# Optimization experiments

Measured on AMD Instinct MI355X. Metric: run time of the kernel, lower is better.

The kernel has to match this reference:

```python
import jax, jax.numpy as jnp
import numpy as np

B, S, H, KV, D, HID = 1, 2048, 32, 8, 128, 4096
SCALE = D ** -0.5
EPS = 1e-5
QMAX = 127.0  # 8-bit symmetric fake quant


def fake_quant(x):
    # per-tensor symmetric int8 fake quantization with straight-through estimator
    s = jnp.maximum(jnp.max(jnp.abs(x)), 1e-5) / QMAX
    q = jnp.clip(jnp.round(x / s), -QMAX - 1.0, QMAX) * s
    return x + jax.lax.stop_gradient(q - x)


def rms_norm(x, w):
    xf = x.astype(jnp.float32)
    var = jnp.mean(xf * xf, axis=-1, keepdims=True)
    return (xf * jax.lax.rsqrt(var + EPS)).astype(x.dtype) * w


def rotate_half(x):
    h = x.shape[-1] // 2
    return jnp.concatenate([-x[..., h:], x[..., :h]], axis=-1)


def qlinear(x, W):
    # QuantLinear: fake-quant activation and weight, then matmul (no bias)
    return fake_quant(x) @ fake_quant(W).T


def setup_inputs() -> dict:
    key = jax.random.key(0)
    ks = jax.random.split(key, 5)
    hidden_states = jax.random.normal(ks[0], (B, S, HID), jnp.float32)
    # RoPE tables
    inv_freq = 1.0 / (10000.0 ** (np.arange(0, D, 2, dtype=np.float32) / D))
    freqs = np.outer(np.arange(S, dtype=np.float32), inv_freq)  # [S, D/2]
    emb = np.concatenate([freqs, freqs], axis=-1)  # [S, D]
    cos = jnp.asarray(np.cos(emb))[None]  # [1,S,D]
    sin = jnp.asarray(np.sin(emb))[None]
    # causal additive mask [1,1,S,S]
    mask = jnp.where(np.tril(np.ones((S, S), dtype=bool)), 0.0, -1e9).astype(jnp.float32)[None, None]
    Wq = jax.random.normal(ks[1], (H * D, HID), jnp.float32) * 0.02
    Wk = jax.random.normal(ks[2], (KV * D, HID), jnp.float32) * 0.02
    Wv = jax.random.normal(ks[3], (KV * D, HID), jnp.float32) * 0.02
    Wo = jax.random.normal(ks[4], (HID, H * D), jnp.float32) * 0.02
    q_norm_w = jnp.ones((D,), jnp.float32)
    k_norm_w = jnp.ones((D,), jnp.float32)
    return dict(hidden_states=hidden_states, cos=cos, sin=sin, attention_mask=mask,
                Wq=Wq, Wk=Wk, Wv=Wv, Wo=Wo, q_norm_w=q_norm_w, k_norm_w=k_norm_w)


def reference(hidden_states, cos, sin, attention_mask, Wq, Wk, Wv, Wo, q_norm_w, k_norm_w):
    b, s, _ = hidden_states.shape
    q = qlinear(hidden_states, Wq).reshape(b, s, H, D).transpose(0, 2, 1, 3)   # [B,H,S,D]
    k = qlinear(hidden_states, Wk).reshape(b, s, KV, D).transpose(0, 2, 1, 3)  # [B,KV,S,D]
    v = qlinear(hidden_states, Wv).reshape(b, s, KV, D).transpose(0, 2, 1, 3)
    q = rms_norm(q, q_norm_w)
    k = rms_norm(k, k_norm_w)
    c = cos[:, None]  # unsqueeze head dim -> [1,1,S,D]
    sn = sin[:, None]
    q = q * c + rotate_half(q) * sn
    k = k * c + rotate_half(k) * sn
    n_rep = H // KV
    k = jnp.repeat(k, n_rep, axis=1)  # [B,H,S,D]
    v = jnp.repeat(v, n_rep, axis=1)
    # fake-quant around QK^T
    q = fake_quant(q)
    k = fake_quant(k)
    scores = jnp.einsum('bhqd,bhkd->bhqk', q, k) * SCALE + attention_mask
    p = jax.nn.softmax(scores.astype(jnp.float32), axis=-1).astype(q.dtype)
    # fake-quant around PV
    p = fake_quant(p)
    v = fake_quant(v)
    out = jnp.einsum('bhqk,bhkd->bhqd', p, v)
    out = out.transpose(0, 2, 1, 3).reshape(b, s, H * D)
    return qlinear(out, Wo)
```

## Files before the change

### kernel.cpp

```cpp
#include <hip/hip_runtime.h>
#include <hip/hip_bf16.h>
#include <math.h>
#include <stdint.h>

#define S_LEN 2048
#define NH    32
#define NKV   8
#define HD    128
#define HIDD  4096

typedef unsigned short u16;
typedef __attribute__((ext_vector_type(4))) int i32x4;

#define GLD16(g, l) __builtin_amdgcn_global_load_lds( \
    (const __attribute__((address_space(1))) void*)(g), \
    (__attribute__((address_space(3))) void*)(l), 16, 0, 0)


__device__ __forceinline__ float slot_scale(const unsigned* slot) {
    return fmaxf(__uint_as_float(*slot), 1e-5f) / 127.0f;
}

__device__ __forceinline__ float exp2_fast(float x) {
    float r; asm("v_exp_f32 %0, %1" : "=v"(r) : "v"(x)); return r;
}
__device__ __forceinline__ float log2_fast(float x) {
    float r; asm("v_log_f32 %0, %1" : "=v"(r) : "v"(x)); return r;
}

__device__ __forceinline__ int qint(float x, float s) {
    float q = rintf(x / s);
    q = fminf(fmaxf(q, -128.0f), 127.0f);
    return (int)q;
}

__device__ __forceinline__ void block_amax_atomic(float m, unsigned* slot) {
    __shared__ float wmax[8];
    const int lane = threadIdx.x & 63;
    const int wid  = threadIdx.x >> 6;
    const int nw   = blockDim.x >> 6;
    #pragma unroll
    for (int o = 32; o; o >>= 1) m = fmaxf(m, __shfl_xor(m, o));
    if (lane == 0) wmax[wid] = m;
    __syncthreads();
    if (threadIdx.x == 0) {
        float bm = wmax[0];
        for (int i = 1; i < nw; ++i) bm = fmaxf(bm, wmax[i]);
        atomicMax(slot, __float_as_uint(bm));
    }
}

struct Amax5Args { const float* p[5]; size_t n4[5]; };
__global__ __launch_bounds__(256) void absmax5_kernel(Amax5Args a, unsigned* slots) {
    const int t = blockIdx.y;
    const float4* x4 = (const float4*)a.p[t];
    const size_t n4 = a.n4[t];
    size_t i = (size_t)blockIdx.x * blockDim.x + threadIdx.x;
    size_t stride = (size_t)gridDim.x * blockDim.x;
    float m = 0.0f;
    for (; i < n4; i += stride) {
        float4 v = x4[i];
        m = fmaxf(m, fmaxf(fmaxf(fabsf(v.x), fabsf(v.y)), fmaxf(fabsf(v.z), fabsf(v.w))));
    }
    block_amax_atomic(m, slots + t);
}

struct Quant5Args { const float* p[5]; char* o[5]; size_t n4[5]; };
__global__ __launch_bounds__(256) void quant5_kernel(Quant5Args a, const unsigned* slots) {
    const int t = blockIdx.y;
    float s = slot_scale(slots + t);
    const float4* x4 = (const float4*)a.p[t];
    unsigned* o4 = (unsigned*)a.o[t];
    const size_t n4 = a.n4[t];
    size_t i = (size_t)blockIdx.x * blockDim.x + threadIdx.x;
    size_t stride = (size_t)gridDim.x * blockDim.x;
    for (; i < n4; i += stride) {
        float4 v = x4[i];
        unsigned o = (unsigned)(qint(v.x, s) & 255)
                   | ((unsigned)(qint(v.y, s) & 255) << 8)
                   | ((unsigned)(qint(v.z, s) & 255) << 16)
                   | ((unsigned)(qint(v.w, s) & 255) << 24);
        o4[i] = o;
    }
}

__global__ __launch_bounds__(256) void quant_kernel(const float* __restrict__ x,
                                                    size_t n4, const unsigned* slot,
                                                    char* __restrict__ out) {
    float s = slot_scale(slot);
    size_t i = (size_t)blockIdx.x * blockDim.x + threadIdx.x;
    size_t stride = (size_t)gridDim.x * blockDim.x;
    const float4* x4 = (const float4*)x;
    unsigned* o4 = (unsigned*)out;
    for (; i < n4; i += stride) {
        float4 v = x4[i];
        unsigned o = (unsigned)(qint(v.x, s) & 255)
                   | ((unsigned)(qint(v.y, s) & 255) << 8)
                   | ((unsigned)(qint(v.z, s) & 255) << 16)
                   | ((unsigned)(qint(v.w, s) & 255) << 24);
        o4[i] = o;
    }
}

__device__ __forceinline__ void gemm_body(const char* __restrict__ A,
                                          const char* __restrict__ B,
                                          float* __restrict__ C,
                                          int m0, int n0, int N, int K,
                                          float scale, unsigned* out_amax,
                                          char* Asm, char* Bsm) {
    const int tid  = threadIdx.x;
    const int lane = tid & 63;
    const int wave = tid >> 6;
    const int wr = (wave >> 1) * 64;
    const int wc = (wave & 1) * 64;
    const int l15 = lane & 15;
    const int l4  = lane >> 4;
    const int cx  = (l4 ^ (l15 & 3)) * 16;
    const int r0  = tid >> 2;
    const int sc  = ((tid & 3) ^ ((tid >> 2) & 3)) * 16;

    i32x4 acc[4][4];
    #pragma unroll
    for (int i = 0; i < 4; ++i)
        #pragma unroll
        for (int j = 0; j < 4; ++j) acc[i][j] = (i32x4){0, 0, 0, 0};

    auto STAGE = [&](int buf, int k0) {
        GLD16(&A[(size_t)(m0 + r0) * K + k0 + sc],      &Asm[buf * 8192 + wave * 1024]);
        GLD16(&A[(size_t)(m0 + 64 + r0) * K + k0 + sc], &Asm[buf * 8192 + 4096 + wave * 1024]);
        GLD16(&B[(size_t)(n0 + r0) * K + k0 + sc],      &Bsm[buf * 8192 + wave * 1024]);
        GLD16(&B[(size_t)(n0 + 64 + r0) * K + k0 + sc], &Bsm[buf * 8192 + 4096 + wave * 1024]);
    };

    STAGE(0, 0);
    __syncthreads();
    int cur = 0;
    const int NT = K >> 6;
    for (int t = 0; t < NT; ++t) {
        if (t + 1 < NT) STAGE(cur ^ 1, (t + 1) << 6);
        i32x4 af[4], bfr[4];
        #pragma unroll
        for (int i = 0; i < 4; ++i)
            af[i] = *(const i32x4*)&Asm[cur * 8192 + (wr + i * 16 + l15) * 64 + cx];
        #pragma unroll
        for (int j = 0; j < 4; ++j)
            bfr[j] = *(const i32x4*)&Bsm[cur * 8192 + (wc + j * 16 + l15) * 64 + cx];
        #pragma unroll
        for (int i = 0; i < 4; ++i)
            #pragma unroll
            for (int j = 0; j < 4; ++j)
                acc[i][j] = __builtin_amdgcn_mfma_i32_16x16x64_i8(af[i], bfr[j], acc[i][j], 0, 0, 0);
        __syncthreads();
        cur ^= 1;
    }

    float lm = 0.0f;
    #pragma unroll
    for (int i = 0; i < 4; ++i)
        #pragma unroll
        for (int j = 0; j < 4; ++j)
            #pragma unroll
            for (int r = 0; r < 4; ++r) {
                int row = m0 + wr + i * 16 + l4 * 4 + r;
                int col = n0 + wc + j * 16 + l15;
                float v = (float)acc[i][j][r] * scale;
                C[(size_t)row * N + col] = v;
                lm = fmaxf(lm, fabsf(v));
            }
    if (out_amax) block_amax_atomic(lm, out_amax);
}

__global__ __launch_bounds__(256) void gemm_qkv_kernel(const char* __restrict__ Aq,
                                                       const char* __restrict__ Wqq,
                                                       const char* __restrict__ Wkq,
                                                       const char* __restrict__ Wvq,
                                                       float* __restrict__ qf,
                                                       float* __restrict__ kf,
                                                       float* __restrict__ vf,
                                                       const unsigned* __restrict__ slots,
                                                       unsigned* v_amax) {
    __shared__ __align__(16) char Asm[2 * 8192];
    __shared__ __align__(16) char Bsm[2 * 8192];
    int bid = blockIdx.x;
    int swz = (bid & 7) * 96 + (bid >> 3);
    int x = swz & 15, y = swz >> 4;
    const char* B; float* C; int N, nb; const unsigned* sB; unsigned* am = nullptr;
    if (y < 32)      { B = Wqq; C = qf; N = NH * HD;  nb = y;      sB = slots + 1; }
    else if (y < 40) { B = Wkq; C = kf; N = NKV * HD; nb = y - 32; sB = slots + 2; }
    else             { B = Wvq; C = vf; N = NKV * HD; nb = y - 40; sB = slots + 3; am = v_amax; }
    float scale = slot_scale(slots + 0) * slot_scale(sB);
    gemm_body(Aq, B, C, x * 128, nb * 128, N, HIDD, scale, am, Asm, Bsm);
}

__global__ __launch_bounds__(256) void gemm_o_kernel(const char* __restrict__ A,
                                                     const char* __restrict__ Woq,
                                                     float* __restrict__ C,
                                                     const unsigned* __restrict__ slots) {
    __shared__ __align__(16) char Asm[2 * 8192];
    __shared__ __align__(16) char Bsm[2 * 8192];
    int bid = blockIdx.x;
    int swz = (bid & 7) * 64 + (bid >> 3);
    int x = swz & 15, y = swz >> 4;
    float scale = slot_scale(slots + 8) * slot_scale(slots + 4);
    gemm_body(A, Woq, C, x * 128, y * 128, NH * HD, HIDD, scale, nullptr, Asm, Bsm);
}

__global__ __launch_bounds__(256) void rmsrope2_kernel(float* __restrict__ qx,
                                                       float* __restrict__ kx,
                                                       const float* __restrict__ cosb,
                                                       const float* __restrict__ sinb,
                                                       const float* __restrict__ qw,
                                                       const float* __restrict__ kw,
                                                       unsigned* slots) {
    const int which = blockIdx.y;
    float* x = which ? kx : qx;
    const float* w = which ? kw : qw;
    const int s_shift = which ? 3 : 5;
    const int nrows = which ? (S_LEN * NKV) : (S_LEN * NH);
    unsigned* slot = slots + (which ? 6 : 5);

    const int lane = threadIdx.x & 63;
    const int wid  = threadIdx.x >> 6;
    const float wa = w[lane];
    const float wb = w[lane + 64];
    float lm = 0.0f;
    for (int row = blockIdx.x * 4 + wid; row < nrows; row += gridDim.x * 4) {
        int s = row >> s_shift;
        float* xr = x + (size_t)row * 128;
        float a = xr[lane], b = xr[lane + 64];
        float ss = a * a + b * b;
        #pragma unroll
        for (int o = 32; o; o >>= 1) ss += __shfl_xor(ss, o);
        float inv = 1.0f / sqrtf(ss * (1.0f / 128.0f) + 1e-5f);
        float ya = (a * inv) * wa;
        float yb = (b * inv) * wb;
        const float* cr = cosb + (size_t)s * 128;
        const float* sr = sinb + (size_t)s * 128;
        float o0 = ya * cr[lane]      - yb * sr[lane];
        float o1 = yb * cr[lane + 64] + ya * sr[lane + 64];
        xr[lane] = o0;
        xr[lane + 64] = o1;
        lm = fmaxf(lm, fmaxf(fabsf(o0), fabsf(o1)));
    }
    block_amax_atomic(lm, slot);
}

__global__ __launch_bounds__(256) void quant_qk2_kernel(const float* __restrict__ qx,
                                                        const float* __restrict__ kx,
                                                        const unsigned* slots,
                                                        char* __restrict__ qq,
                                                        char* __restrict__ kq) {
    int tid = blockIdx.x * 256 + threadIdx.x;
    const int qtot = S_LEN * NH * HD;
    if (tid < qtot) {
        float s = slot_scale(slots + 5);
        int d  = tid & 127;
        int h  = (tid >> 7) & 31;
        int sp = tid >> 12;
        qq[((size_t)h * S_LEN + sp) * 128 + d] = (char)qint(qx[tid], s);
    } else {
        tid -= qtot;
        float s = slot_scale(slots + 6);
        int d  = tid & 127;
        int h  = (tid >> 7) & 7;
        int sp = tid >> 10;
        kq[((size_t)h * S_LEN + sp) * 128 + d] = (char)qint(kx[tid], s);
    }
}

__global__ __launch_bounds__(256) void quant_v_kernel(const float* __restrict__ x,
                                                      const unsigned* slot,
                                                      char* __restrict__ out) {
    __shared__ unsigned char t8[64][36];
    const float s = slot_scale(slot);
    const int t   = threadIdx.x;
    const int sp0 = blockIdx.x * 64;
    const int d0  = blockIdx.y * 32;
    const int kvh = blockIdx.z;
    const int dl = t & 31;
    const int sb = t >> 5;
    #pragma unroll
    for (int j = 0; j < 8; ++j) {
        int spl = sb + j * 8;
        float v = x[((size_t)(sp0 + spl) * NKV + kvh) * 128 + d0 + dl];
        t8[spl][dl] = (unsigned char)qint(v, s);
    }
    __syncthreads();
    const int dd = t >> 3;
    const int ch = t & 7;
    unsigned lo = 0, hi = 0;
    #pragma unroll
    for (int j = 0; j < 4; ++j) lo |= (unsigned)t8[ch * 8 + j][dd] << (8 * j);
    #pragma unroll
    for (int j = 0; j < 4; ++j) hi |= (unsigned)t8[ch * 8 + 4 + j][dd] << (8 * j);
    *(uint2*)&out[((size_t)kvh * 128 + d0 + dd) * S_LEN + sp0 + ch * 8] = make_uint2(lo, hi);
}

__global__ __launch_bounds__(256) void attn_kernel(const char* __restrict__ Qq,
                                                   const char* __restrict__ Kq,
                                                   const char* __restrict__ Vt,
                                                   const unsigned* sq_slot,
                                                   const unsigned* sk_slot,
                                                   const unsigned* sv_slot,
                                                   float* __restrict__ O,
                                                   unsigned* amax_slot) {
    __shared__ __align__(16) char Klds[64 * 144];
    __shared__ __align__(16) char Vlds[128 * 80];
    __shared__ __align__(16) char pldsB[4][16 * 80];
    __shared__ __align__(16) char pldsS[4][16 * 80];

    const int tid  = threadIdx.x;
    const int lane = tid & 63;
    const int wave = tid >> 6;
    const int h  = blockIdx.y;
    const int kv = h >> 2;
    const int l15 = lane & 15;
    const int l4  = lane >> 4;
    const size_t kvS = (size_t)kv * S_LEN;

    const int qtS = blockIdx.x;
    const int qtB = 31 - qtS;
    const int qr0S = qtS * 64 + wave * 16;
    const int qr0B = qtB * 64 + wave * 16;

    const float sq = slot_scale(sq_slot);
    const float sk = slot_scale(sk_slot);
    const float sv = slot_scale(sv_slot);
    const float qs2 = sq * sk * 0.08838834764831845f * 1.4426950408889634f;
    const float osc = (1.0f / 127.0f) * sv;
    const float NEG = -1e30f;

    i32x4 qfS[2], qfB[2];
    {
        const char* qpS = Qq + ((size_t)h * S_LEN + qr0S + l15) * 128 + l4 * 16;
        const char* qpB = Qq + ((size_t)h * S_LEN + qr0B + l15) * 128 + l4 * 16;
        qfS[0] = *(const i32x4*)(qpS); qfS[1] = *(const i32x4*)(qpS + 64);
        qfB[0] = *(const i32x4*)(qpB); qfB[1] = *(const i32x4*)(qpB + 64);
    }

    auto qk_block = [&](int hb, const i32x4* qf2) -> i32x4 {
        i32x4 sacc = {0, 0, 0, 0};
        #pragma unroll
        for (int c = 0; c < 2; ++c) {
            i32x4 kfa = *(const i32x4*)&Klds[(hb * 16 + l15) * 144 + c * 64 + l4 * 16];
            sacc = __builtin_amdgcn_mfma_i32_16x16x64_i8(kfa, qf2[c], sacc, 0, 0, 0);
        }
        return sacc;
    };

    float mS = NEG, lS = 0.0f, mB = NEG, lB = 0.0f;

    auto p1_interior = [&](int hb, const i32x4* qf2, float& m_l, float& l_l) {
        i32x4 sacc = qk_block(hb, qf2);
        float x0 = (float)sacc[0] * qs2, x1 = (float)sacc[1] * qs2;
        float x2 = (float)sacc[2] * qs2, x3 = (float)sacc[3] * qs2;
        float bm = fmaxf(fmaxf(x0, x1), fmaxf(x2, x3));
        float mn = fmaxf(m_l, bm);
        float ps = exp2_fast(x0 - mn) + exp2_fast(x1 - mn)
                 + exp2_fast(x2 - mn) + exp2_fast(x3 - mn);
        l_l = l_l * exp2_fast(m_l - mn) + ps;
        m_l = mn;
    };
    auto p1_diag = [&](int hb, const i32x4* qf2, float& m_l, float& l_l) {
        i32x4 sacc = qk_block(hb, qf2);
        float x[4];
        #pragma unroll
        for (int r = 0; r < 4; ++r) {
            float v = (float)sacc[r] * qs2;
            x[r] = ((l4 * 4 + r) > l15) ? NEG : v;
        }
        float bm = fmaxf(fmaxf(x[0], x[1]), fmaxf(x[2], x[3]));
        float mn = fmaxf(m_l, bm);
        float ps = exp2_fast(x[0] - mn) + exp2_fast(x[1] - mn)
                 + exp2_fast(x[2] - mn) + exp2_fast(x[3] - mn);
        l_l = l_l * exp2_fast(m_l - mn) + ps;
        m_l = mn;
    };

    i32x4 kreg[2];
    #pragma unroll
    for (int c = 0; c < 2; ++c) {
        int idx = c * 256 + tid;
        kreg[c] = *(const i32x4*)&Kq[(kvS + (idx >> 3)) * 128 + (idx & 7) * 16];
    }
    #pragma unroll 1
    for (int kc = 0; kc <= qtB; ++kc) {
        __syncthreads();
        #pragma unroll
        for (int c = 0; c < 2; ++c) {
            int idx = c * 256 + tid;
            *(i32x4*)&Klds[(idx >> 3) * 144 + (idx & 7) * 16] = kreg[c];
        }
        __syncthreads();
        if (kc < qtB) {
            #pragma unroll
            for (int c = 0; c < 2; ++c) {
                int idx = c * 256 + tid;
                kreg[c] = *(const i32x4*)&Kq[(kvS + (kc + 1) * 64 + (idx >> 3)) * 128 + (idx & 7) * 16];
            }
        }
        if (kc < qtB) {
            p1_interior(0, qfB, mB, lB); p1_interior(1, qfB, mB, lB);
            p1_interior(2, qfB, mB, lB); p1_interior(3, qfB, mB, lB);
        } else {
            #pragma unroll
            for (int hb = 0; hb < 4; ++hb) {
                if (hb < wave) p1_interior(hb, qfB, mB, lB);
                else if (hb == wave) p1_diag(hb, qfB, mB, lB);
            }
        }
        if (kc < qtS) {
            p1_interior(0, qfS, mS, lS); p1_interior(1, qfS, mS, lS);
            p1_interior(2, qfS, mS, lS); p1_interior(3, qfS, mS, lS);
        } else if (kc == qtS) {
            #pragma unroll
            for (int hb = 0; hb < 4; ++hb) {
                if (hb < wave) p1_interior(hb, qfS, mS, lS);
                else if (hb == wave) p1_diag(hb, qfS, mS, lS);
            }
        }
    }
    auto merge = [&](float m_l, float l_l) -> float2 {
        float m2 = fmaxf(m_l, __shfl_xor(m_l, 16));
        float mfin = fmaxf(m2, __shfl_xor(m2, 32));
        float t = l_l * exp2_fast(m_l - mfin);
        t += __shfl_xor(t, 16);
        t += __shfl_xor(t, 32);
        return make_float2(mfin, mfin - log2_fast(127.0f / t));
    };
    float2 mcS = merge(mS, lS);
    float2 mcB = merge(mB, lB);
    const float cS = mcS.y, cB = mcB.y;

    i32x4 oaccS[8], oaccB[8];
    #pragma unroll
    for (int dt = 0; dt < 8; ++dt) {
        oaccS[dt] = (i32x4){0, 0, 0, 0};
        oaccB[dt] = (i32x4){0, 0, 0, 0};
    }

    auto p2_interior = [&](int hb, const i32x4* qf2, float c) -> unsigned {
        i32x4 sacc = qk_block(hb, qf2);
        unsigned pack = 0;
        #pragma unroll
        for (int r = 0; r < 4; ++r) {
            float pq = rintf(exp2_fast((float)sacc[r] * qs2 - c));
            pack |= ((unsigned)(int)pq) << (8 * r);
        }
        return pack;
    };
    auto p2_diag = [&](int hb, const i32x4* qf2, float c) -> unsigned {
        i32x4 sacc = qk_block(hb, qf2);
        unsigned pack = 0;
        #pragma unroll
        for (int r = 0; r < 4; ++r) {
            float p = exp2_fast((float)sacc[r] * qs2 - c);
            float pq = ((l4 * 4 + r) > l15) ? 0.0f : rintf(p);
            pack |= ((unsigned)(int)pq) << (8 * r);
        }
        return pack;
    };
    auto pv8 = [&](char (*plds)[16 * 80], i32x4* oacc) {
        i32x4 pf = *(const i32x4*)&plds[wave][l15 * 80 + l4 * 16];
        #pragma unroll
        for (int dt = 0; dt < 8; ++dt) {
            i32x4 vfb = *(const i32x4*)&Vlds[(dt * 16 + l15) * 80 + l4 * 16];
            oacc[dt] = __builtin_amdgcn_mfma_i32_16x16x64_i8(pf, vfb, oacc[dt], 0, 0, 0);
        }
    };

    i32x4 vreg[2];
    #pragma unroll
    for (int c = 0; c < 2; ++c) {
        int idx = c * 256 + tid;
        kreg[c] = *(const i32x4*)&Kq[(kvS + (idx >> 3)) * 128 + (idx & 7) * 16];
        vreg[c] = *(const i32x4*)&Vt[((size_t)kv * 128 + (idx >> 2)) * S_LEN + (idx & 3) * 16];
    }
    #pragma unroll 1
    for (int kc = 0; kc <= qtB; ++kc) {
        __syncthreads();
        #pragma unroll
        for (int c = 0; c < 2; ++c) {
            int idx = c * 256 + tid;
            *(i32x4*)&Klds[(idx >> 3) * 144 + (idx & 7) * 16] = kreg[c];
            *(i32x4*)&Vlds[(idx >> 2) * 80 + (idx & 3) * 16] = vreg[c];
        }
        __syncthreads();
        if (kc < qtB) {
            #pragma unroll
            for (int c = 0; c < 2; ++c) {
                int idx = c * 256 + tid;
                kreg[c] = *(const i32x4*)&Kq[(kvS + (kc + 1) * 64 + (idx >> 3)) * 128 + (idx & 7) * 16];
                vreg[c] = *(const i32x4*)&Vt[((size_t)kv * 128 + (idx >> 2)) * S_LEN + (kc + 1) * 64 + (idx & 3) * 16];
            }
        }
        if (kc < qtB) {
            #pragma unroll
            for (int hb = 0; hb < 4; ++hb)
                *(unsigned*)&pldsB[wave][l15 * 80 + hb * 16 + l4 * 4] = p2_interior(hb, qfB, cB);
        } else {
            #pragma unroll
            for (int hb = 0; hb < 4; ++hb) {
                unsigned pack = 0;
                if (hb < wave) pack = p2_interior(hb, qfB, cB);
                else if (hb == wave) pack = p2_diag(hb, qfB, cB);
                *(unsigned*)&pldsB[wave][l15 * 80 + hb * 16 + l4 * 4] = pack;
            }
        }
        pv8(pldsB, oaccB);
        if (kc < qtS) {
            #pragma unroll
            for (int hb = 0; hb < 4; ++hb)
                *(unsigned*)&pldsS[wave][l15 * 80 + hb * 16 + l4 * 4] = p2_interior(hb, qfS, cS);
            pv8(pldsS, oaccS);
        } else if (kc == qtS) {
            #pragma unroll
            for (int hb = 0; hb < 4; ++hb) {
                unsigned pack = 0;
                if (hb < wave) pack = p2_interior(hb, qfS, cS);
                else if (hb == wave) pack = p2_diag(hb, qfS, cS);
                *(unsigned*)&pldsS[wave][l15 * 80 + hb * 16 + l4 * 4] = pack;
            }
            pv8(pldsS, oaccS);
        }
    }

    float lm = 0.0f;
    #pragma unroll
    for (int dt = 0; dt < 8; ++dt)
        #pragma unroll
        for (int r = 0; r < 4; ++r) {
            float vB = (float)oaccB[dt][r] * osc;
            float vS = (float)oaccS[dt][r] * osc;
            int col = h * 128 + dt * 16 + l15;
            O[(size_t)(qr0B + l4 * 4 + r) * (NH * 128) + col] = vB;
            O[(size_t)(qr0S + l4 * 4 + r) * (NH * 128) + col] = vS;
            lm = fmaxf(lm, fmaxf(fabsf(vB), fabsf(vS)));
        }
    block_amax_atomic(lm, amax_slot);
}

extern "C" void kernel_launch(void* const* d_in, const int* in_sizes, int n_in,
                              void* d_out, int out_size, void* d_ws, size_t ws_size,
                              hipStream_t stream) {
    const float* hs   = (const float*)d_in[0];
    const float* cosb = (const float*)d_in[1];
    const float* sinb = (const float*)d_in[2];
    const float* Wq   = (const float*)d_in[4];
    const float* Wk   = (const float*)d_in[5];
    const float* Wv   = (const float*)d_in[6];
    const float* Wo   = (const float*)d_in[7];
    const float* qnw  = (const float*)d_in[8];
    const float* knw  = (const float*)d_in[9];
    float* out = (float*)d_out;

    char* ws = (char*)d_ws;
    unsigned* slots = (unsigned*)ws;
    size_t off = 256;
    auto take = [&](size_t bytes) { size_t o = off; off += (bytes + 255) & ~(size_t)255; return o; };
    char*  hsq  = (char*)(ws + take((size_t)S_LEN * HIDD));
    char*  Wqq  = (char*)(ws + take((size_t)NH * HD * HIDD));
    char*  Wkq  = (char*)(ws + take((size_t)NKV * HD * HIDD));
    char*  Wvq  = (char*)(ws + take((size_t)NKV * HD * HIDD));
    char*  Woq  = (char*)(ws + take((size_t)HIDD * NH * HD));
    float* qf   = (float*)(ws + take((size_t)S_LEN * NH * HD * 4));
    float* kf   = (float*)(ws + take((size_t)S_LEN * NKV * HD * 4));
    float* vf   = (float*)(ws + take((size_t)S_LEN * NKV * HD * 4));
    char*  qq   = (char*)(ws + take((size_t)NH * S_LEN * HD));
    char*  kq   = (char*)(ws + take((size_t)NKV * S_LEN * HD));
    char*  vtq  = (char*)(ws + take((size_t)NKV * HD * S_LEN));
    float* attnf = qf;
    char*  attnq = hsq;

    hipMemsetAsync(ws, 0, 64, stream);

    const size_t n_hs = (size_t)S_LEN * HIDD;
    const size_t n_wq = (size_t)NH * HD * HIDD;
    const size_t n_wk = (size_t)NKV * HD * HIDD;

    Amax5Args aa;
    aa.p[0] = hs; aa.p[1] = Wq; aa.p[2] = Wk; aa.p[3] = Wv; aa.p[4] = Wo;
    aa.n4[0] = n_hs / 4; aa.n4[1] = n_wq / 4; aa.n4[2] = n_wk / 4;
    aa.n4[3] = n_wk / 4; aa.n4[4] = n_wq / 4;
    absmax5_kernel<<<dim3(512, 5), 256, 0, stream>>>(aa, slots);

    Quant5Args qa;
    qa.p[0] = hs; qa.p[1] = Wq; qa.p[2] = Wk; qa.p[3] = Wv; qa.p[4] = Wo;
    qa.o[0] = hsq; qa.o[1] = Wqq; qa.o[2] = Wkq; qa.o[3] = Wvq; qa.o[4] = Woq;
    qa.n4[0] = n_hs / 4; qa.n4[1] = n_wq / 4; qa.n4[2] = n_wk / 4;
    qa.n4[3] = n_wk / 4; qa.n4[4] = n_wq / 4;
    quant5_kernel<<<dim3(1024, 5), 256, 0, stream>>>(qa, slots);

    gemm_qkv_kernel<<<768, 256, 0, stream>>>(hsq, Wqq, Wkq, Wvq, qf, kf, vf,
                                             slots, slots + 7);

    rmsrope2_kernel<<<dim3(1024, 2), 256, 0, stream>>>(qf, kf, cosb, sinb, qnw, knw, slots);

    quant_qk2_kernel<<<40960, 256, 0, stream>>>(qf, kf, slots, qq, kq);
    quant_v_kernel<<<dim3(32, 4, 8), 256, 0, stream>>>(vf, slots + 7, vtq);

    attn_kernel<<<dim3(16, NH), 256, 0, stream>>>(qq, kq, vtq,
                                                  slots + 5, slots + 6, slots + 7,
                                                  attnf, slots + 8);

    quant_kernel<<<2048, 256, 0, stream>>>(attnf, n_hs / 4, slots + 8, attnq);
    gemm_o_kernel<<<512, 256, 0, stream>>>(attnq, Woq, out, slots);
    (void)in_sizes; (void)n_in; (void)out_size; (void)ws_size;
}
```

Before: 363.1 us.

## Triple-buffer int8 GEMM LDS staging with vmcnt waits; raise priority in PV MFMA

The int8 GEMM mainloop moves from double to triple buffering. It prefetches two K-tiles ahead and uses explicit s_waitcnt vmcnt plus a single s_barrier per iteration instead of two __syncthreads, so more global-to-LDS load latency is hidden. The attention kernel fuses the score scale-and-subtract into an fmaf and raises wave priority around the PV MFMA loop. The cost is 50% more LDS per GEMM block, which may lower occupancy, and the correctness of the vmcnt(4) count relies on exactly four loads per stage.

```diff
diff --git a/kernel.cpp b/kernel.cpp
--- a/kernel.cpp
+++ b/kernel.cpp
@@ -132,12 +132,23 @@
         GLD16(&B[(size_t)(n0 + 64 + r0) * K + k0 + sc], &Bsm[buf * 8192 + 4096 + wave * 1024]);
     };
 
+    const int NT = K >> 6;
     STAGE(0, 0);
-    __syncthreads();
+    STAGE(1, 64);
     int cur = 0;
-    const int NT = K >> 6;
     for (int t = 0; t < NT; ++t) {
-        if (t + 1 < NT) STAGE(cur ^ 1, (t + 1) << 6);
+        if (t + 1 < NT) {
+            asm volatile("s_waitcnt vmcnt(4)" ::: "memory");
+        } else {
+            asm volatile("s_waitcnt vmcnt(0)" ::: "memory");
+        }
+        __builtin_amdgcn_sched_barrier(0);
+        __builtin_amdgcn_s_barrier();
+        __builtin_amdgcn_sched_barrier(0);
+        if (t + 2 < NT) {
+            int nb = cur + 2; if (nb >= 3) nb -= 3;
+            STAGE(nb, (t + 2) << 6);
+        }
         i32x4 af[4], bfr[4];
         #pragma unroll
         for (int i = 0; i < 4; ++i)
@@ -150,8 +161,7 @@
             #pragma unroll
             for (int j = 0; j < 4; ++j)
                 acc[i][j] = __builtin_amdgcn_mfma_i32_16x16x64_i8(af[i], bfr[j], acc[i][j], 0, 0, 0);
-        __syncthreads();
-        cur ^= 1;
+        cur += 1; if (cur == 3) cur = 0;
     }
 
     float lm = 0.0f;
@@ -167,6 +177,7 @@
                 C[(size_t)row * N + col] = v;
                 lm = fmaxf(lm, fabsf(v));
             }
+    __syncthreads();
     if (out_amax) block_amax_atomic(lm, out_amax);
 }
 
@@ -179,8 +190,8 @@
                                                        float* __restrict__ vf,
                                                        const unsigned* __restrict__ slots,
                                                        unsigned* v_amax) {
-    __shared__ __align__(16) char Asm[2 * 8192];
-    __shared__ __align__(16) char Bsm[2 * 8192];
+    __shared__ __align__(16) char Asm[3 * 8192];
+    __shared__ __align__(16) char Bsm[3 * 8192];
     int bid = blockIdx.x;
     int swz = (bid & 7) * 96 + (bid >> 3);
     int x = swz & 15, y = swz >> 4;
@@ -196,8 +207,8 @@
                                                      const char* __restrict__ Woq,
                                                      float* __restrict__ C,
                                                      const unsigned* __restrict__ slots) {
-    __shared__ __align__(16) char Asm[2 * 8192];
-    __shared__ __align__(16) char Bsm[2 * 8192];
+    __shared__ __align__(16) char Asm[3 * 8192];
+    __shared__ __align__(16) char Bsm[3 * 8192];
     int bid = blockIdx.x;
     int swz = (bid & 7) * 64 + (bid >> 3);
     int x = swz & 15, y = swz >> 4;
@@ -420,17 +431,16 @@
             }
         }
     }
-    auto merge = [&](float m_l, float l_l) -> float2 {
+    auto merge = [&](float m_l, float l_l) -> float {
         float m2 = fmaxf(m_l, __shfl_xor(m_l, 16));
         float mfin = fmaxf(m2, __shfl_xor(m2, 32));
         float t = l_l * exp2_fast(m_l - mfin);
         t += __shfl_xor(t, 16);
         t += __shfl_xor(t, 32);
-        return make_float2(mfin, mfin - log2_fast(127.0f / t));
-    };
-    float2 mcS = merge(mS, lS);
-    float2 mcB = merge(mB, lB);
-    const float cS = mcS.y, cB = mcB.y;
+        return mfin - log2_fast(127.0f / t);
+    };
+    const float cS = merge(mS, lS);
+    const float cB = merge(mB, lB);
 
     i32x4 oaccS[8], oaccB[8];
     #pragma unroll
@@ -444,7 +454,7 @@
         unsigned pack = 0;
         #pragma unroll
         for (int r = 0; r < 4; ++r) {
-            float pq = rintf(exp2_fast((float)sacc[r] * qs2 - c));
+            float pq = rintf(exp2_fast(fmaf((float)sacc[r], qs2, -c)));
             pack |= ((unsigned)(int)pq) << (8 * r);
         }
         return pack;
@@ -454,7 +464,7 @@
         unsigned pack = 0;
         #pragma unroll
         for (int r = 0; r < 4; ++r) {
-            float p = exp2_fast((float)sacc[r] * qs2 - c);
+            float p = exp2_fast(fmaf((float)sacc[r], qs2, -c));
             float pq = ((l4 * 4 + r) > l15) ? 0.0f : rintf(p);
             pack |= ((unsigned)(int)pq) << (8 * r);
         }
@@ -462,11 +472,13 @@
     };
     auto pv8 = [&](char (*plds)[16 * 80], i32x4* oacc) {
         i32x4 pf = *(const i32x4*)&plds[wave][l15 * 80 + l4 * 16];
+        __builtin_amdgcn_s_setprio(1);
         #pragma unroll
         for (int dt = 0; dt < 8; ++dt) {
             i32x4 vfb = *(const i32x4*)&Vlds[(dt * 16 + l15) * 80 + l4 * 16];
             oacc[dt] = __builtin_amdgcn_mfma_i32_16x16x64_i8(pf, vfb, oacc[dt], 0, 0, 0);
         }
+        __builtin_amdgcn_s_setprio(0);
     };
 
     i32x4 vreg[2];
```

New measurement: 355.2 us. 1.02x faster.

## Split-K the int8 GEMMs with atomic accumulation and move V amax into rmsrope

Applied to the files above, without the earlier changes.

Both quantized GEMMs now split the K dimension in two and double their block count. Partial results are accumulated into fp32 outputs with atomicAdd, and those outputs are zeroed by extra memsets beforehand. The aim is more parallel work and better CU occupancy on the QKV and O projections. Because the GEMM epilogue can no longer compute the V abs-max, that reduction moves into a third slice of the rmsrope kernel. Minor attention tweaks are added too: FMA in the exp argument and raised wave priority around the PV MFMAs. The cost is extra memset traffic, atomic read-modify-write traffic and nondeterministic summation order.

```diff
diff --git a/kernel.cpp b/kernel.cpp
--- a/kernel.cpp
+++ b/kernel.cpp
@@ -102,10 +102,11 @@
     }
 }
 
+template<bool ATOMIC>
 __device__ __forceinline__ void gemm_body(const char* __restrict__ A,
                                           const char* __restrict__ B,
                                           float* __restrict__ C,
-                                          int m0, int n0, int N, int K,
+                                          int m0, int n0, int N, int kbeg, int kend,
                                           float scale, unsigned* out_amax,
                                           char* Asm, char* Bsm) {
     const int tid  = threadIdx.x;
@@ -126,18 +127,18 @@
         for (int j = 0; j < 4; ++j) acc[i][j] = (i32x4){0, 0, 0, 0};
 
     auto STAGE = [&](int buf, int k0) {
-        GLD16(&A[(size_t)(m0 + r0) * K + k0 + sc],      &Asm[buf * 8192 + wave * 1024]);
-        GLD16(&A[(size_t)(m0 + 64 + r0) * K + k0 + sc], &Asm[buf * 8192 + 4096 + wave * 1024]);
-        GLD16(&B[(size_t)(n0 + r0) * K + k0 + sc],      &Bsm[buf * 8192 + wave * 1024]);
-        GLD16(&B[(size_t)(n0 + 64 + r0) * K + k0 + sc], &Bsm[buf * 8192 + 4096 + wave * 1024]);
-    };
-
-    STAGE(0, 0);
+        GLD16(&A[(size_t)(m0 + r0) * HIDD + k0 + sc],      &Asm[buf * 8192 + wave * 1024]);
+        GLD16(&A[(size_t)(m0 + 64 + r0) * HIDD + k0 + sc], &Asm[buf * 8192 + 4096 + wave * 1024]);
+        GLD16(&B[(size_t)(n0 + r0) * HIDD + k0 + sc],      &Bsm[buf * 8192 + wave * 1024]);
+        GLD16(&B[(size_t)(n0 + 64 + r0) * HIDD + k0 + sc], &Bsm[buf * 8192 + 4096 + wave * 1024]);
+    };
+
+    const int NT = (kend - kbeg) >> 6;
+    STAGE(0, kbeg);
     __syncthreads();
     int cur = 0;
-    const int NT = K >> 6;
     for (int t = 0; t < NT; ++t) {
-        if (t + 1 < NT) STAGE(cur ^ 1, (t + 1) << 6);
+        if (t + 1 < NT) STAGE(cur ^ 1, kbeg + ((t + 1) << 6));
         i32x4 af[4], bfr[4];
         #pragma unroll
         for (int i = 0; i < 4; ++i)
@@ -164,55 +165,78 @@
                 int row = m0 + wr + i * 16 + l4 * 4 + r;
                 int col = n0 + wc + j * 16 + l15;
                 float v = (float)acc[i][j][r] * scale;
-                C[(size_t)row * N + col] = v;
-                lm = fmaxf(lm, fabsf(v));
+                if (ATOMIC) {
+                    atomicAdd(&C[(size_t)row * N + col], v);
+                } else {
+                    C[(size_t)row * N + col] = v;
+                    lm = fmaxf(lm, fabsf(v));
+                }
             }
-    if (out_amax) block_amax_atomic(lm, out_amax);
-}
-
-__global__ __launch_bounds__(256) void gemm_qkv_kernel(const char* __restrict__ Aq,
-                                                       const char* __restrict__ Wqq,
-                                                       const char* __restrict__ Wkq,
-                                                       const char* __restrict__ Wvq,
-                                                       float* __restrict__ qf,
-                                                       float* __restrict__ kf,
-                                                       float* __restrict__ vf,
-                                                       const unsigned* __restrict__ slots,
-                                                       unsigned* v_amax) {
+    if (!ATOMIC && out_amax) block_amax_atomic(lm, out_amax);
+}
+
+__global__ __launch_bounds__(256, 4) void gemm_qkv_kernel(const char* __restrict__ Aq,
+                                                          const char* __restrict__ Wqq,
+                                                          const char* __restrict__ Wkq,
+                                                          const char* __restrict__ Wvq,
+                                                          float* __restrict__ qf,
+                                                          float* __restrict__ kf,
+                                                          float* __restrict__ vf,
+                                                          const unsigned* __restrict__ slots) {
     __shared__ __align__(16) char Asm[2 * 8192];
     __shared__ __align__(16) char Bsm[2 * 8192];
     int bid = blockIdx.x;
-    int swz = (bid & 7) * 96 + (bid >> 3);
-    int x = swz & 15, y = swz >> 4;
-    const char* B; float* C; int N, nb; const unsigned* sB; unsigned* am = nullptr;
+    int swz = (bid & 7) * 192 + (bid >> 3);
+    int kh  = swz / 768;
+    int rem = swz - kh * 768;
+    int x = rem & 15, y = rem >> 4;
+    const char* B; float* C; int N, nb; const unsigned* sB;
     if (y < 32)      { B = Wqq; C = qf; N = NH * HD;  nb = y;      sB = slots + 1; }
     else if (y < 40) { B = Wkq; C = kf; N = NKV * HD; nb = y - 32; sB = slots + 2; }
-    else             { B = Wvq; C = vf; N = NKV * HD; nb = y - 40; sB = slots + 3; am = v_amax; }
+    else             { B = Wvq; C = vf; N = NKV * HD; nb = y - 40; sB = slots + 3; }
     float scale = slot_scale(slots + 0) * slot_scale(sB);
-    gemm_body(Aq, B, C, x * 128, nb * 128, N, HIDD, scale, am, Asm, Bsm);
-}
-
-__global__ __launch_bounds__(256) void gemm_o_kernel(const char* __restrict__ A,
-                                                     const char* __restrict__ Woq,
-                                                     float* __restrict__ C,
-                                                     const unsigned* __restrict__ slots) {
+    gemm_body<true>(Aq, B, C, x * 128, nb * 128, N, kh * 2048, kh * 2048 + 2048,
+                    scale, nullptr, Asm, Bsm);
+}
+
+__global__ __launch_bounds__(256, 4) void gemm_o_kernel(const char* __restrict__ A,
+                                                        const char* __restrict__ Woq,
+                                                        float* __restrict__ C,
+                                                        const unsigned* __restrict__ slots) {
     __shared__ __align__(16) char Asm[2 * 8192];
     __shared__ __align__(16) char Bsm[2 * 8192];
     int bid = blockIdx.x;
-    int swz = (bid & 7) * 64 + (bid >> 3);
-    int x = swz & 15, y = swz >> 4;
+    int swz = (bid & 7) * 128 + (bid >> 3);
+    int kh  = swz >> 9;
+    int rem = swz & 511;
+    int x = rem & 15, y = rem >> 4;
     float scale = slot_scale(slots + 8) * slot_scale(slots + 4);
-    gemm_body(A, Woq, C, x * 128, y * 128, NH * HD, HIDD, scale, nullptr, Asm, Bsm);
+    gemm_body<true>(A, Woq, C, x * 128, y * 128, NH * HD, kh * 2048, kh * 2048 + 2048,
+                    scale, nullptr, Asm, Bsm);
 }
 
 __global__ __launch_bounds__(256) void rmsrope2_kernel(float* __restrict__ qx,
                                                        float* __restrict__ kx,
+                                                       const float* __restrict__ vx,
                                                        const float* __restrict__ cosb,
                                                        const float* __restrict__ sinb,
                                                        const float* __restrict__ qw,
                                                        const float* __restrict__ kw,
                                                        unsigned* slots) {
     const int which = blockIdx.y;
+    if (which == 2) {
+        const float4* x4 = (const float4*)vx;
+        const size_t n4 = (size_t)S_LEN * NKV * HD / 4;
+        size_t i = (size_t)blockIdx.x * blockDim.x + threadIdx.x;
+        size_t stride = (size_t)gridDim.x * blockDim.x;
+        float m = 0.0f;
+        for (; i < n4; i += stride) {
+            float4 v = x4[i];
+            m = fmaxf(m, fmaxf(fmaxf(fabsf(v.x), fabsf(v.y)), fmaxf(fabsf(v.z), fabsf(v.w))));
+        }
+        block_amax_atomic(m, slots + 7);
+        return;
+    }
     float* x = which ? kx : qx;
     const float* w = which ? kw : qw;
     const int s_shift = which ? 3 : 5;
@@ -420,17 +444,16 @@
             }
         }
     }
-    auto merge = [&](float m_l, float l_l) -> float2 {
+    auto merge = [&](float m_l, float l_l) -> float {
         float m2 = fmaxf(m_l, __shfl_xor(m_l, 16));
         float mfin = fmaxf(m2, __shfl_xor(m2, 32));
         float t = l_l * exp2_fast(m_l - mfin);
         t += __shfl_xor(t, 16);
         t += __shfl_xor(t, 32);
-        return make_float2(mfin, mfin - log2_fast(127.0f / t));
-    };
-    float2 mcS = merge(mS, lS);
-    float2 mcB = merge(mB, lB);
-    const float cS = mcS.y, cB = mcB.y;
+        return mfin - log2_fast(127.0f / t);
+    };
+    const float cS = merge(mS, lS);
+    const float cB = merge(mB, lB);
 
     i32x4 oaccS[8], oaccB[8];
     #pragma unroll
@@ -444,7 +467,7 @@
         unsigned pack = 0;
         #pragma unroll
         for (int r = 0; r < 4; ++r) {
-            float pq = rintf(exp2_fast((float)sacc[r] * qs2 - c));
+            float pq = rintf(exp2_fast(fmaf((float)sacc[r], qs2, -c)));
             pack |= ((unsigned)(int)pq) << (8 * r);
         }
         return pack;
@@ -454,7 +477,7 @@
         unsigned pack = 0;
         #pragma unroll
         for (int r = 0; r < 4; ++r) {
-            float p = exp2_fast((float)sacc[r] * qs2 - c);
+            float p = exp2_fast(fmaf((float)sacc[r], qs2, -c));
             float pq = ((l4 * 4 + r) > l15) ? 0.0f : rintf(p);
             pack |= ((unsigned)(int)pq) << (8 * r);
         }
@@ -462,11 +485,13 @@
     };
     auto pv8 = [&](char (*plds)[16 * 80], i32x4* oacc) {
         i32x4 pf = *(const i32x4*)&plds[wave][l15 * 80 + l4 * 16];
+        __builtin_amdgcn_s_setprio(1);
         #pragma unroll
         for (int dt = 0; dt < 8; ++dt) {
             i32x4 vfb = *(const i32x4*)&Vlds[(dt * 16 + l15) * 80 + l4 * 16];
             oacc[dt] = __builtin_amdgcn_mfma_i32_16x16x64_i8(pf, vfb, oacc[dt], 0, 0, 0);
         }
+        __builtin_amdgcn_s_setprio(0);
     };
 
     i32x4 vreg[2];
@@ -573,6 +598,7 @@
     char*  attnq = hsq;
 
     hipMemsetAsync(ws, 0, 64, stream);
+    hipMemsetAsync(qf, 0, (size_t)S_LEN * NH * HD * 4 + 2 * (size_t)S_LEN * NKV * HD * 4, stream);
 
     const size_t n_hs = (size_t)S_LEN * HIDD;
     const size_t n_wq = (size_t)NH * HD * HIDD;
@@ -591,19 +617,20 @@
     qa.n4[3] = n_wk / 4; qa.n4[4] = n_wq / 4;
     quant5_kernel<<<dim3(1024, 5), 256, 0, stream>>>(qa, slots);
 
-    gemm_qkv_kernel<<<768, 256, 0, stream>>>(hsq, Wqq, Wkq, Wvq, qf, kf, vf,
-                                             slots, slots + 7);
-
-    rmsrope2_kernel<<<dim3(1024, 2), 256, 0, stream>>>(qf, kf, cosb, sinb, qnw, knw, slots);
+    gemm_qkv_kernel<<<1536, 256, 0, stream>>>(hsq, Wqq, Wkq, Wvq, qf, kf, vf, slots);
+
+    rmsrope2_kernel<<<dim3(1024, 3), 256, 0, stream>>>(qf, kf, vf, cosb, sinb, qnw, knw, slots);
 
     quant_qk2_kernel<<<40960, 256, 0, stream>>>(qf, kf, slots, qq, kq);
     quant_v_kernel<<<dim3(32, 4, 8), 256, 0, stream>>>(vf, slots + 7, vtq);
+
+    hipMemsetAsync(d_out, 0, (size_t)S_LEN * NH * HD * 4, stream);
 
     attn_kernel<<<dim3(16, NH), 256, 0, stream>>>(qq, kq, vtq,
                                                   slots + 5, slots + 6, slots + 7,
                                                   attnf, slots + 8);
 
     quant_kernel<<<2048, 256, 0, stream>>>(attnf, n_hs / 4, slots + 8, attnq);
-    gemm_o_kernel<<<512, 256, 0, stream>>>(attnq, Woq, out, slots);
+    gemm_o_kernel<<<1024, 256, 0, stream>>>(attnq, Woq, out, slots);
     (void)in_sizes; (void)n_in; (void)out_size; (void)ws_size;
 }
```

Result: slower. 445.1 us (+22.6%).
